# Performance work log

Hardware: AMD Instinct MI355X
Metric: run time of the kernel (lower is better)

## Reference

```python
import jax, jax.numpy as jnp
import numpy as np

B, S_ENC, S_DEC = 256, 1024, 1024
IN, H, OUT = 100, 128, 200
G = 4 * H  # PyTorch LSTM gate rows (i, f, g, o)


def setup_inputs() -> dict:
    key = jax.random.key(0)
    keys = iter(jax.random.split(key, 32))
    w = 1.0 / np.sqrt(H)  # mimic PyTorch LSTM init scale

    def rn(shape, s):
        return jax.random.normal(next(keys), shape, dtype=jnp.float32) * s

    return {
        "x": rn((B, S_ENC, IN), 1.0),
        "y": rn((B, S_DEC, OUT), 1.0),
        "enc_Wih0": rn((G, IN), w), "enc_Whh0": rn((G, H), w),
        "enc_bih0": rn((G,), w), "enc_bhh0": rn((G,), w),
        "enc_Wih1": rn((G, H), w), "enc_Whh1": rn((G, H), w),
        "enc_bih1": rn((G,), w), "enc_bhh1": rn((G,), w),
        "dec_Wih0": rn((G, OUT), w), "dec_Whh0": rn((G, H), w),
        "dec_bih0": rn((G,), w), "dec_bhh0": rn((G,), w),
        "dec_Wih1": rn((G, H), w), "dec_Whh1": rn((G, H), w),
        "dec_bih1": rn((G,), w), "dec_bhh1": rn((G,), w),
        "fc_W": rn((OUT, H), w), "fc_b": rn((OUT,), w),
    }


def lstm_layer(x, h0, c0, Wih, Whh, bih, bhh):
    """Single LSTM layer over full sequence. x: [B,S,D_in] -> [B,S,H], (hT,cT).
    PyTorch gate order: i, f, g, o."""
    # Precompute input projections for all timesteps in one GEMM: [B,S,4H]
    x_proj = jnp.einsum('bsd,gd->bsg', x, Wih) + bih + bhh

    def step(carry, xp_t):
        h, c = carry
        gates = xp_t + h @ Whh.T  # [B,4H]
        i, f, g, o = jnp.split(gates, 4, axis=-1)
        i, f, o = jax.nn.sigmoid(i), jax.nn.sigmoid(f), jax.nn.sigmoid(o)
        g = jnp.tanh(g)
        c = f * c + i * g
        h = o * jnp.tanh(c)
        return (h, c), h

    (hT, cT), hs = jax.lax.scan(step, (h0, c0), x_proj.transpose(1, 0, 2))
    return hs.transpose(1, 0, 2), hT, cT


def lstm_2layer(x, h0_stack, c0_stack, p0, p1):
    """2-layer LSTM. h0_stack/c0_stack: [2,B,H]. p0/p1: (Wih,Whh,bih,bhh)."""
    out0, h0T, c0T = lstm_layer(x, h0_stack[0], c0_stack[0], *p0)
    out1, h1T, c1T = lstm_layer(out0, h0_stack[1], c0_stack[1], *p1)
    hn = jnp.stack([h0T, h1T])
    cn = jnp.stack([c0T, c1T])
    return out1, hn, cn


def reference(x, y,
              enc_Wih0, enc_Whh0, enc_bih0, enc_bhh0,
              enc_Wih1, enc_Whh1, enc_bih1, enc_bhh1,
              dec_Wih0, dec_Whh0, dec_bih0, dec_bhh0,
              dec_Wih1, dec_Whh1, dec_bih1, dec_bhh1,
              fc_W, fc_b):
    b = x.shape[0]
    z = jnp.zeros((2, b, H), dtype=x.dtype)
    # Encoder: zero init state
    _, hn, cn = lstm_2layer(
        x, z, z,
        (enc_Wih0, enc_Whh0, enc_bih0, enc_bhh0),
        (enc_Wih1, enc_Whh1, enc_bih1, enc_bhh1))
    # Teacher-forced decoder: input at step i is y[:, i-1, :], zeros at i=0
    dec_in = jnp.concatenate(
        [jnp.zeros((b, 1, OUT), dtype=y.dtype), y[:, :-1, :]], axis=1)
    dec_out, _, _ = lstm_2layer(
        dec_in, hn, cn,
        (dec_Wih0, dec_Whh0, dec_bih0, dec_bhh0),
        (dec_Wih1, dec_Whh1, dec_bih1, dec_bhh1))
    # Per-step Linear == one batched GEMM over the sequence
    return jnp.einsum('bsh,oh->bso', dec_out, fc_W) + fc_b
```

## Files before the change

kernel.cpp:

```cpp
#include <hip/hip_runtime.h>

#define NB 256
#define HH 128
#define GG 512

#define BM 128
#define BN 128
#define KS 16
#define LPITCH 132

__global__ __launch_bounds__(256, 2) void proj_gemm(
    const float* __restrict__ A, long long lda_b, long long lda_t, int t00, int tsh,
    const float* __restrict__ W,
    const float* __restrict__ b1, const float* __restrict__ b2,
    float* __restrict__ C, long long ldc_b, long long ldc_t, int tC0,
    int CH, int K, int N)
{
  __shared__ float As[KS * LPITCH];
  __shared__ float Ws[KS * LPITCH];

  const int tid = threadIdx.x;
  const int tx = tid & 15;
  const int ty = tid >> 4;

  const long long row0 = (long long)blockIdx.x * BM;
  const int nbase = blockIdx.y * BN;

  const int lr  = tid >> 1;
  const int lks = (tid & 1) * 8;
  const long long lrow = row0 + lr;
  const int lb  = (int)(lrow / CH);
  const int lti = (int)(lrow - (long long)lb * CH);
  const int lt  = t00 + lti + tsh;
  const float* Arow = (lt >= 0) ? (A + (long long)lb * lda_b + (long long)lt * lda_t)
                                : (const float*)nullptr;
  const int ln = nbase + lr;
  const float* Wrow = (ln < N) ? (W + (long long)ln * K) : (const float*)nullptr;

  float acc[8][8];
#pragma unroll
  for (int i = 0; i < 8; ++i)
#pragma unroll
    for (int j = 0; j < 8; ++j) acc[i][j] = 0.f;

  const int nS = (K + KS - 1) / KS;

  float4 ra0 = make_float4(0.f,0.f,0.f,0.f), ra1 = ra0, rw0 = ra0, rw1 = ra0;

  auto loadRegs = [&](int s) {
    const int k0 = s * KS + lks;
    const float4 z = make_float4(0.f, 0.f, 0.f, 0.f);
    ra0 = (Arow && (k0 + 4 <= K)) ? *(const float4*)(Arow + k0)     : z;
    ra1 = (Arow && (k0 + 8 <= K)) ? *(const float4*)(Arow + k0 + 4) : z;
    rw0 = (Wrow && (k0 + 4 <= K)) ? *(const float4*)(Wrow + k0)     : z;
    rw1 = (Wrow && (k0 + 8 <= K)) ? *(const float4*)(Wrow + k0 + 4) : z;
  };

  loadRegs(0);

  for (int s = 0; s < nS; ++s) {
    __syncthreads();
    {
      float av[8] = {ra0.x, ra0.y, ra0.z, ra0.w, ra1.x, ra1.y, ra1.z, ra1.w};
      float wv[8] = {rw0.x, rw0.y, rw0.z, rw0.w, rw1.x, rw1.y, rw1.z, rw1.w};
#pragma unroll
      for (int j = 0; j < 8; ++j) {
        As[(lks + j) * LPITCH + lr] = av[j];
        Ws[(lks + j) * LPITCH + lr] = wv[j];
      }
    }
    __syncthreads();
    if (s + 1 < nS) loadRegs(s + 1);

#pragma unroll
    for (int kk = 0; kk < KS; ++kk) {
      const float* ar = &As[kk * LPITCH];
      const float* wr = &Ws[kk * LPITCH];
      float4 A0 = *(const float4*)(ar + ty * 8);
      float4 A1 = *(const float4*)(ar + ty * 8 + 4);
      float4 W0 = *(const float4*)(wr + tx * 4);
      float4 W1 = *(const float4*)(wr + 64 + tx * 4);
      float am[8] = {A0.x, A0.y, A0.z, A0.w, A1.x, A1.y, A1.z, A1.w};
      float wm[8] = {W0.x, W0.y, W0.z, W0.w, W1.x, W1.y, W1.z, W1.w};
#pragma unroll
      for (int i = 0; i < 8; ++i)
#pragma unroll
        for (int j = 0; j < 8; ++j)
          acc[i][j] = fmaf(am[i], wm[j], acc[i][j]);
    }
  }

  const bool fullN = (nbase + BN <= N);
#pragma unroll
  for (int i = 0; i < 8; ++i) {
    long long row = row0 + ty * 8 + i;
    int bb = (int)(row / CH);
    int ti = (int)(row - (long long)bb * CH);
    float* crow = C + (long long)bb * ldc_b + (long long)(tC0 + ti) * ldc_t;
    if (fullN) {
      int c0 = nbase + tx * 4;
      int c1 = nbase + 64 + tx * 4;
      const float4 bv0 = *(const float4*)(b1 + c0);
      const float4 bv1 = *(const float4*)(b1 + c1);
      float4 v0 = make_float4(acc[i][0] + bv0.x, acc[i][1] + bv0.y,
                              acc[i][2] + bv0.z, acc[i][3] + bv0.w);
      float4 v1 = make_float4(acc[i][4] + bv1.x, acc[i][5] + bv1.y,
                              acc[i][6] + bv1.z, acc[i][7] + bv1.w);
      if (b2) {
        const float4 c20 = *(const float4*)(b2 + c0);
        const float4 c21 = *(const float4*)(b2 + c1);
        v0.x += c20.x; v0.y += c20.y; v0.z += c20.z; v0.w += c20.w;
        v1.x += c21.x; v1.y += c21.y; v1.z += c21.z; v1.w += c21.w;
      }
      *(float4*)(crow + c0) = v0;
      *(float4*)(crow + c1) = v1;
    } else {
#pragma unroll
      for (int j = 0; j < 8; ++j) {
        int col = nbase + ((j < 4) ? (tx * 4 + j) : (64 + tx * 4 + (j - 4)));
        if (col < N) {
          float bv = b1[col];
          if (b2) bv += b2[col];
          crow[col] = acc[i][j] + bv;
        }
      }
    }
  }
}

__device__ __forceinline__ float rl(float v, int l) {
  return __int_as_float(__builtin_amdgcn_readlane(__float_as_int(v), l));
}
__device__ __forceinline__ void barrier_lgkm() {
  asm volatile("s_waitcnt lgkmcnt(0)\n\ts_barrier" ::: "memory");
}
__device__ __forceinline__ float sigm_fast(float x) {
  float e = __expf(-x);
  return __builtin_amdgcn_rcpf(1.f + e);
}
__device__ __forceinline__ float tanh_fast(float x) {
  float e = __expf(2.f * x);
  return fmaf(-2.f, __builtin_amdgcn_rcpf(e + 1.f), 1.f);
}

__global__ __launch_bounds__(512, 2) void lstm_rec(
    const float* __restrict__ xp,
    const float* __restrict__ Whh,
    float* __restrict__ h_state,
    float* __restrict__ c_state,
    float* __restrict__ out_seq,
    int CH, int init)
{
  __shared__ float act_lds[2][GG + 8];

  const int g = threadIdx.x;
  const int b = blockIdx.x;
  const int lane = g & 63;

  float4 w[32];
  {
    const float4* wr4 = (const float4*)(Whh + (long long)g * HH);
#pragma unroll
    for (int i = 0; i < 32; ++i) w[i] = wr4[i];
  }

  float2 hv, cv;
  if (init) {
    hv = make_float2(0.f, 0.f); cv = make_float2(0.f, 0.f);
  } else {
    hv = *(const float2*)&h_state[b * HH + 2 * lane];
    cv = *(const float2*)&c_state[b * HH + 2 * lane];
  }

  const float* xpb = xp + (long long)b * CH * GG + g;
  float xv0 = xpb[0];
  float xv1 = (CH > 1) ? xpb[GG] : 0.f;
  float xv2 = (CH > 2) ? xpb[2 * GG] : 0.f;

  for (int t = 0; t < CH; ++t) {
    float xv3 = (t + 3 < CH) ? xpb[(long long)(t + 3) * GG] : 0.f;

    float a0 = xv0, a1 = 0.f, a2 = 0.f, a3 = 0.f;
#pragma unroll
    for (int q = 0; q < 32; ++q) {
      const float4 wq = w[q];
      const int l0 = 2 * q, l1 = 2 * q + 1;
      a0 = fmaf(rl(hv.x, l0), wq.x, a0);
      a1 = fmaf(rl(hv.y, l0), wq.y, a1);
      a2 = fmaf(rl(hv.x, l1), wq.z, a2);
      a3 = fmaf(rl(hv.y, l1), wq.w, a3);
    }
    const float gate = (a0 + a1) + (a2 + a3);

    const int buf = t & 1;
    const float act = (g >= 2 * HH && g < 3 * HH) ? tanh_fast(gate)
                                                  : sigm_fast(gate);
    act_lds[buf][g + 2 * (g >> 7)] = act;

    barrier_lgkm();

    const int e = 2 * lane;
    const float2 iv = *(const float2*)&act_lds[buf][e];
    const float2 fv = *(const float2*)&act_lds[buf][e + HH + 2];
    const float2 gv = *(const float2*)&act_lds[buf][e + 2 * HH + 4];
    const float2 ov = *(const float2*)&act_lds[buf][e + 3 * HH + 6];
    cv.x = fmaf(fv.x, cv.x, iv.x * gv.x);
    cv.y = fmaf(fv.y, cv.y, iv.y * gv.y);
    hv.x = ov.x * tanh_fast(cv.x);
    hv.y = ov.y * tanh_fast(cv.y);

    if (out_seq && g < 64)
      *(float2*)&out_seq[(long long)b * CH * HH + (long long)t * HH + e] = hv;

    xv0 = xv1; xv1 = xv2; xv2 = xv3;
  }

  if (g < 64) {
    *(float2*)&h_state[b * HH + 2 * lane] = hv;
    *(float2*)&c_state[b * HH + 2 * lane] = cv;
  }
}

extern "C" void kernel_launch(void* const* d_in, const int* in_sizes, int n_in,
                              void* d_out, int out_size, void* d_ws, size_t ws_size,
                              hipStream_t stream)
{
  (void)in_sizes; (void)n_in; (void)out_size;

  const float* x     = (const float*)d_in[0];
  const float* y     = (const float*)d_in[1];
  const float* eWih0 = (const float*)d_in[2];
  const float* eWhh0 = (const float*)d_in[3];
  const float* ebih0 = (const float*)d_in[4];
  const float* ebhh0 = (const float*)d_in[5];
  const float* eWih1 = (const float*)d_in[6];
  const float* eWhh1 = (const float*)d_in[7];
  const float* ebih1 = (const float*)d_in[8];
  const float* ebhh1 = (const float*)d_in[9];
  const float* dWih0 = (const float*)d_in[10];
  const float* dWhh0 = (const float*)d_in[11];
  const float* dbih0 = (const float*)d_in[12];
  const float* dbhh0 = (const float*)d_in[13];
  const float* dWih1 = (const float*)d_in[14];
  const float* dWhh1 = (const float*)d_in[15];
  const float* dbih1 = (const float*)d_in[16];
  const float* dbhh1 = (const float*)d_in[17];
  const float* fcW   = (const float*)d_in[18];
  const float* fcb   = (const float*)d_in[19];
  float* out = (float*)d_out;

  const int S = 1024;

  int CH = 16;
  {
    const int cands[5] = {256, 128, 64, 32, 16};
    for (int i = 0; i < 5; ++i) {
      long long need = (long long)NB * cands[i] * 4LL * (GG + HH + HH)
                     + 4LL * NB * HH * 4
                     + 4096;
      if (need <= (long long)ws_size) { CH = cands[i]; break; }
    }
  }
  const int nchunks = S / CH;

  float* xpb  = (float*)d_ws;
  float* seqA = xpb  + (long long)NB * CH * GG;
  float* seqB = seqA + (long long)NB * CH * HH;
  float* h0s  = seqB + (long long)NB * CH * HH;
  float* c0s  = h0s + NB * HH;
  float* h1s  = c0s + NB * HH;
  float* c1s  = h1s + NB * HH;

  dim3 pgrid((NB * CH) / BM, GG / BN);
  dim3 fgrid((NB * CH) / BM, (200 + BN - 1) / BN);
  dim3 pblk(256);
  dim3 rgrid(NB);
  dim3 rblk(512);

  for (int cidx = 0; cidx < nchunks; ++cidx) {
    int t0 = cidx * CH;
    proj_gemm<<<pgrid, pblk, 0, stream>>>(
        x, (long long)S * 100, 100, t0, 0,
        eWih0, ebih0, ebhh0,
        xpb, (long long)CH * GG, GG, 0, CH, 100, GG);
    lstm_rec<<<rgrid, rblk, 0, stream>>>(xpb, eWhh0, h0s, c0s, seqA, CH, cidx == 0 ? 1 : 0);
    proj_gemm<<<pgrid, pblk, 0, stream>>>(
        seqA, (long long)CH * HH, HH, 0, 0,
        eWih1, ebih1, ebhh1,
        xpb, (long long)CH * GG, GG, 0, CH, HH, GG);
    lstm_rec<<<rgrid, rblk, 0, stream>>>(xpb, eWhh1, h1s, c1s, (float*)nullptr, CH, cidx == 0 ? 1 : 0);
  }

  for (int cidx = 0; cidx < nchunks; ++cidx) {
    int t0 = cidx * CH;
    proj_gemm<<<pgrid, pblk, 0, stream>>>(
        y, (long long)S * 200, 200, t0, -1,
        dWih0, dbih0, dbhh0,
        xpb, (long long)CH * GG, GG, 0, CH, 200, GG);
    lstm_rec<<<rgrid, rblk, 0, stream>>>(xpb, dWhh0, h0s, c0s, seqA, CH, 0);
    proj_gemm<<<pgrid, pblk, 0, stream>>>(
        seqA, (long long)CH * HH, HH, 0, 0,
        dWih1, dbih1, dbhh1,
        xpb, (long long)CH * GG, GG, 0, CH, HH, GG);
    lstm_rec<<<rgrid, rblk, 0, stream>>>(xpb, dWhh1, h1s, c1s, seqB, CH, 0);
    proj_gemm<<<fgrid, pblk, 0, stream>>>(
        seqB, (long long)CH * HH, HH, 0, 0,
        fcW, fcb, (const float*)nullptr,
        out, (long long)S * 200, 200, t0, CH, HH, 200);
  }
}
```

Measured before the change: 9.060 ms.

## Use split-bf16 MFMA for LSTM recurrence with 16 batch rows per block

Replaces the per-batch FP32 readlane/FMA recurrence with a kernel where each block handles 16 batch rows and computes h@Whh^T using bf16 MFMA instructions. The hi/lo bf16 splitting of weights and hidden state (three MFMAs per tile) keeps the result close to fp32. Weights are pre-split once per launch by a small conversion kernel. The hidden state is exchanged through double-buffered LDS. The trade-off is fewer blocks (16 instead of 256), so fewer CUs are used, plus extra split work and some loss of precision.

New measurement: 10.57 ms. 1.17x slower.

```diff
diff --git a/kernel.cpp b/kernel.cpp
--- a/kernel.cpp
+++ b/kernel.cpp
@@ -3,6 +3,9 @@
 #define NB 256
 #define HH 128
 #define GG 512
+
+typedef __attribute__((ext_vector_type(8))) short bf8;
+typedef __attribute__((ext_vector_type(4))) float f32x4;
 
 #define BM 128
 #define BN 128
@@ -128,9 +131,27 @@
   }
 }
 
-__device__ __forceinline__ float rl(float v, int l) {
-  return __int_as_float(__builtin_amdgcn_readlane(__float_as_int(v), l));
-}
+__device__ __forceinline__ unsigned short f2bf(float f) {
+  unsigned int u = __float_as_uint(f);
+  return (unsigned short)((u + 0x7fffu + ((u >> 16) & 1u)) >> 16);
+}
+__device__ __forceinline__ float bf2f(unsigned short h) {
+  return __uint_as_float(((unsigned int)h) << 16);
+}
+
+__global__ void split_bf16(const float* __restrict__ src,
+                           unsigned short* __restrict__ hi,
+                           unsigned short* __restrict__ lo, int n)
+{
+  int i = blockIdx.x * blockDim.x + threadIdx.x;
+  if (i < n) {
+    float v = src[i];
+    unsigned short h = f2bf(v);
+    hi[i] = h;
+    lo[i] = f2bf(v - bf2f(h));
+  }
+}
+
 __device__ __forceinline__ void barrier_lgkm() {
   asm volatile("s_waitcnt lgkmcnt(0)\n\ts_barrier" ::: "memory");
 }
@@ -143,81 +164,153 @@
   return fmaf(-2.f, __builtin_amdgcn_rcpf(e + 1.f), 1.f);
 }
 
-__global__ __launch_bounds__(512, 2) void lstm_rec(
+#define HP 136
+
+__global__ __launch_bounds__(256, 1) void lstm_rec_mfma(
     const float* __restrict__ xp,
-    const float* __restrict__ Whh,
+    const unsigned short* __restrict__ whi,
+    const unsigned short* __restrict__ wlo,
     float* __restrict__ h_state,
     float* __restrict__ c_state,
     float* __restrict__ out_seq,
     int CH, int init)
 {
-  __shared__ float act_lds[2][GG + 8];
-
-  const int g = threadIdx.x;
-  const int b = blockIdx.x;
-  const int lane = g & 63;
-
-  float4 w[32];
-  {
-    const float4* wr4 = (const float4*)(Whh + (long long)g * HH);
-#pragma unroll
-    for (int i = 0; i < 32; ++i) w[i] = wr4[i];
-  }
-
-  float2 hv, cv;
+  __shared__ unsigned short hbuf[2][2][16][HP];
+
+  const int tid  = threadIdx.x;
+  const int lane = tid & 63;
+  const int w    = tid >> 6;
+  const int g4   = lane >> 4;
+  const int bl   = lane & 15;
+  const int bb   = blockIdx.x * 16 + bl;
+  const int hwb  = w * 32 + 4 * g4;
+
+  bf8 WH[8][4], WL[8][4];
+#pragma unroll
+  for (int m = 0; m < 8; ++m) {
+    const int T = m >> 1, s = m & 1;
+    const int grow = T * 128 + w * 32 + s * 16 + bl;
+    const unsigned short* rh = whi + grow * 128 + 4 * g4;
+    const unsigned short* rl = wlo + grow * 128 + 4 * g4;
+#pragma unroll
+    for (int kt = 0; kt < 4; ++kt) {
+      ushort4 a0 = *(const ushort4*)(rh + 32 * kt);
+      ushort4 a1 = *(const ushort4*)(rh + 32 * kt + 16);
+      WH[m][kt] = (bf8){(short)a0.x,(short)a0.y,(short)a0.z,(short)a0.w,
+                        (short)a1.x,(short)a1.y,(short)a1.z,(short)a1.w};
+      ushort4 b0 = *(const ushort4*)(rl + 32 * kt);
+      ushort4 b1 = *(const ushort4*)(rl + 32 * kt + 16);
+      WL[m][kt] = (bf8){(short)b0.x,(short)b0.y,(short)b0.z,(short)b0.w,
+                        (short)b1.x,(short)b1.y,(short)b1.z,(short)b1.w};
+    }
+  }
+
+  float cst[8], hs[8];
   if (init) {
-    hv = make_float2(0.f, 0.f); cv = make_float2(0.f, 0.f);
+#pragma unroll
+    for (int i = 0; i < 8; ++i) { cst[i] = 0.f; hs[i] = 0.f; }
   } else {
-    hv = *(const float2*)&h_state[b * HH + 2 * lane];
-    cv = *(const float2*)&c_state[b * HH + 2 * lane];
-  }
-
-  const float* xpb = xp + (long long)b * CH * GG + g;
-  float xv0 = xpb[0];
-  float xv1 = (CH > 1) ? xpb[GG] : 0.f;
-  float xv2 = (CH > 2) ? xpb[2 * GG] : 0.f;
+#pragma unroll
+    for (int s = 0; s < 2; ++s) {
+      float4 cv = *(const float4*)&c_state[bb * HH + hwb + s * 16];
+      float4 hv = *(const float4*)&h_state[bb * HH + hwb + s * 16];
+      cst[s*4+0]=cv.x; cst[s*4+1]=cv.y; cst[s*4+2]=cv.z; cst[s*4+3]=cv.w;
+      hs [s*4+0]=hv.x; hs [s*4+1]=hv.y; hs [s*4+2]=hv.z; hs [s*4+3]=hv.w;
+    }
+  }
+#pragma unroll
+  for (int s = 0; s < 2; ++s) {
+    ushort4 hi4, lo4;
+    unsigned short h0=f2bf(hs[s*4+0]), h1=f2bf(hs[s*4+1]),
+                   h2=f2bf(hs[s*4+2]), h3=f2bf(hs[s*4+3]);
+    hi4 = (ushort4){h0,h1,h2,h3};
+    lo4 = (ushort4){f2bf(hs[s*4+0]-bf2f(h0)), f2bf(hs[s*4+1]-bf2f(h1)),
+                    f2bf(hs[s*4+2]-bf2f(h2)), f2bf(hs[s*4+3]-bf2f(h3))};
+    *(ushort4*)&hbuf[0][0][bl][hwb + s * 16] = hi4;
+    *(ushort4*)&hbuf[0][1][bl][hwb + s * 16] = lo4;
+  }
+  barrier_lgkm();
+
+  const float* xpt = xp + (long long)bb * CH * GG + w * 32 + 4 * g4;
+  f32x4 xpr[8];
+#pragma unroll
+  for (int m = 0; m < 8; ++m)
+    xpr[m] = *(const f32x4*)(xpt + (m >> 1) * 128 + (m & 1) * 16);
+
+  float* osq = out_seq ? (out_seq + (long long)bb * CH * HH + hwb) : (float*)nullptr;
 
   for (int t = 0; t < CH; ++t) {
-    float xv3 = (t + 3 < CH) ? xpb[(long long)(t + 3) * GG] : 0.f;
-
-    float a0 = xv0, a1 = 0.f, a2 = 0.f, a3 = 0.f;
-#pragma unroll
-    for (int q = 0; q < 32; ++q) {
-      const float4 wq = w[q];
-      const int l0 = 2 * q, l1 = 2 * q + 1;
-      a0 = fmaf(rl(hv.x, l0), wq.x, a0);
-      a1 = fmaf(rl(hv.y, l0), wq.y, a1);
-      a2 = fmaf(rl(hv.x, l1), wq.z, a2);
-      a3 = fmaf(rl(hv.y, l1), wq.w, a3);
-    }
-    const float gate = (a0 + a1) + (a2 + a3);
-
     const int buf = t & 1;
-    const float act = (g >= 2 * HH && g < 3 * HH) ? tanh_fast(gate)
-                                                  : sigm_fast(gate);
-    act_lds[buf][g + 2 * (g >> 7)] = act;
-
+
+    bf8 BH[4], BL[4];
+    const unsigned short* hbH = &hbuf[buf][0][bl][4 * g4];
+    const unsigned short* hbL = &hbuf[buf][1][bl][4 * g4];
+#pragma unroll
+    for (int kt = 0; kt < 4; ++kt) {
+      ushort4 a0 = *(const ushort4*)(hbH + 32 * kt);
+      ushort4 a1 = *(const ushort4*)(hbH + 32 * kt + 16);
+      BH[kt] = (bf8){(short)a0.x,(short)a0.y,(short)a0.z,(short)a0.w,
+                     (short)a1.x,(short)a1.y,(short)a1.z,(short)a1.w};
+      ushort4 b0 = *(const ushort4*)(hbL + 32 * kt);
+      ushort4 b1 = *(const ushort4*)(hbL + 32 * kt + 16);
+      BL[kt] = (bf8){(short)b0.x,(short)b0.y,(short)b0.z,(short)b0.w,
+                     (short)b1.x,(short)b1.y,(short)b1.z,(short)b1.w};
+    }
+
+    f32x4 acc[8];
+#pragma unroll
+    for (int m = 0; m < 8; ++m) acc[m] = xpr[m];
+    if (t + 1 < CH) {
+      const float* xpn = xpt + 512;
+#pragma unroll
+      for (int m = 0; m < 8; ++m)
+        xpr[m] = *(const f32x4*)(xpn + (m >> 1) * 128 + (m & 1) * 16);
+    }
+
+#pragma unroll
+    for (int m = 0; m < 8; ++m)
+#pragma unroll
+      for (int kt = 0; kt < 4; ++kt) {
+        acc[m] = __builtin_amdgcn_mfma_f32_16x16x32_bf16(WH[m][kt], BH[kt], acc[m], 0, 0, 0);
+        acc[m] = __builtin_amdgcn_mfma_f32_16x16x32_bf16(WL[m][kt], BH[kt], acc[m], 0, 0, 0);
+        acc[m] = __builtin_amdgcn_mfma_f32_16x16x32_bf16(WH[m][kt], BL[kt], acc[m], 0, 0, 0);
+      }
+
+#pragma unroll
+    for (int s = 0; s < 2; ++s) {
+#pragma unroll
+      for (int r = 0; r < 4; ++r) {
+        float iv = sigm_fast(acc[0 + s][r]);
+        float fv = sigm_fast(acc[2 + s][r]);
+        float gv = tanh_fast(acc[4 + s][r]);
+        float ov = sigm_fast(acc[6 + s][r]);
+        float c  = fmaf(fv, cst[s * 4 + r], iv * gv);
+        cst[s * 4 + r] = c;
+        hs[s * 4 + r]  = ov * tanh_fast(c);
+      }
+      if (osq) {
+        f32x4 h4 = {hs[s*4+0], hs[s*4+1], hs[s*4+2], hs[s*4+3]};
+        *(f32x4*)(osq + (long long)t * HH + s * 16) = h4;
+      }
+      unsigned short h0=f2bf(hs[s*4+0]), h1=f2bf(hs[s*4+1]),
+                     h2=f2bf(hs[s*4+2]), h3=f2bf(hs[s*4+3]);
+      ushort4 hi4 = (ushort4){h0,h1,h2,h3};
+      ushort4 lo4 = (ushort4){f2bf(hs[s*4+0]-bf2f(h0)), f2bf(hs[s*4+1]-bf2f(h1)),
+                              f2bf(hs[s*4+2]-bf2f(h2)), f2bf(hs[s*4+3]-bf2f(h3))};
+      *(ushort4*)&hbuf[buf ^ 1][0][bl][hwb + s * 16] = hi4;
+      *(ushort4*)&hbuf[buf ^ 1][1][bl][hwb + s * 16] = lo4;
+    }
+
+    xpt += 512;
     barrier_lgkm();
-
-    const int e = 2 * lane;
-    const float2 iv = *(const float2*)&act_lds[buf][e];
-    const float2 fv = *(const float2*)&act_lds[buf][e + HH + 2];
-    const float2 gv = *(const float2*)&act_lds[buf][e + 2 * HH + 4];
-    const float2 ov = *(const float2*)&act_lds[buf][e + 3 * HH + 6];
-    cv.x = fmaf(fv.x, cv.x, iv.x * gv.x);
-    cv.y = fmaf(fv.y, cv.y, iv.y * gv.y);
-    hv.x = ov.x * tanh_fast(cv.x);
-    hv.y = ov.y * tanh_fast(cv.y);
-
-    if (out_seq && g < 64)
-      *(float2*)&out_seq[(long long)b * CH * HH + (long long)t * HH + e] = hv;
-
-    xv0 = xv1; xv1 = xv2; xv2 = xv3;
-  }
-
-  if (g < 64) {
-    *(float2*)&h_state[b * HH + 2 * lane] = hv;
-    *(float2*)&c_state[b * HH + 2 * lane] = cv;
+  }
+
+#pragma unroll
+  for (int s = 0; s < 2; ++s) {
+    f32x4 c4 = {cst[s*4+0], cst[s*4+1], cst[s*4+2], cst[s*4+3]};
+    f32x4 h4 = {hs[s*4+0], hs[s*4+1], hs[s*4+2], hs[s*4+3]};
+    *(f32x4*)&c_state[bb * HH + hwb + s * 16] = c4;
+    *(f32x4*)&h_state[bb * HH + hwb + s * 16] = h4;
   }
 }
 
@@ -250,6 +343,8 @@
   float* out = (float*)d_out;
 
   const int S = 1024;
+  const long long WN = (long long)GG * HH;
+  const long long WSPLIT_BYTES = 4 * 2 * WN * 2;
 
   int CH = 16;
   {
@@ -257,7 +352,7 @@
     for (int i = 0; i < 5; ++i) {
       long long need = (long long)NB * cands[i] * 4LL * (GG + HH + HH)
                      + 4LL * NB * HH * 4
-                     + 4096;
+                     + WSPLIT_BYTES + 4096;
       if (need <= (long long)ws_size) { CH = cands[i]; break; }
     }
   }
@@ -270,12 +365,25 @@
   float* c0s  = h0s + NB * HH;
   float* h1s  = c0s + NB * HH;
   float* c1s  = h1s + NB * HH;
+  unsigned short* wsp = (unsigned short*)(c1s + NB * HH);
+  unsigned short* eW0hi = wsp;             unsigned short* eW0lo = wsp + WN;
+  unsigned short* eW1hi = wsp + 2 * WN;    unsigned short* eW1lo = wsp + 3 * WN;
+  unsigned short* dW0hi = wsp + 4 * WN;    unsigned short* dW0lo = wsp + 5 * WN;
+  unsigned short* dW1hi = wsp + 6 * WN;    unsigned short* dW1lo = wsp + 7 * WN;
+
+  {
+    dim3 pg((WN + 255) / 256), pb(256);
+    split_bf16<<<pg, pb, 0, stream>>>(eWhh0, eW0hi, eW0lo, (int)WN);
+    split_bf16<<<pg, pb, 0, stream>>>(eWhh1, eW1hi, eW1lo, (int)WN);
+    split_bf16<<<pg, pb, 0, stream>>>(dWhh0, dW0hi, dW0lo, (int)WN);
+    split_bf16<<<pg, pb, 0, stream>>>(dWhh1, dW1hi, dW1lo, (int)WN);
+  }
 
   dim3 pgrid((NB * CH) / BM, GG / BN);
   dim3 fgrid((NB * CH) / BM, (200 + BN - 1) / BN);
   dim3 pblk(256);
-  dim3 rgrid(NB);
-  dim3 rblk(512);
+  dim3 rgrid(NB / 16);
+  dim3 rblk(256);
 
   for (int cidx = 0; cidx < nchunks; ++cidx) {
     int t0 = cidx * CH;
@@ -283,12 +391,12 @@
         x, (long long)S * 100, 100, t0, 0,
         eWih0, ebih0, ebhh0,
         xpb, (long long)CH * GG, GG, 0, CH, 100, GG);
-    lstm_rec<<<rgrid, rblk, 0, stream>>>(xpb, eWhh0, h0s, c0s, seqA, CH, cidx == 0 ? 1 : 0);
+    lstm_rec_mfma<<<rgrid, rblk, 0, stream>>>(xpb, eW0hi, eW0lo, h0s, c0s, seqA, CH, cidx == 0 ? 1 : 0);
     proj_gemm<<<pgrid, pblk, 0, stream>>>(
         seqA, (long long)CH * HH, HH, 0, 0,
         eWih1, ebih1, ebhh1,
         xpb, (long long)CH * GG, GG, 0, CH, HH, GG);
-    lstm_rec<<<rgrid, rblk, 0, stream>>>(xpb, eWhh1, h1s, c1s, (float*)nullptr, CH, cidx == 0 ? 1 : 0);
+    lstm_rec_mfma<<<rgrid, rblk, 0, stream>>>(xpb, eW1hi, eW1lo, h1s, c1s, (float*)nullptr, CH, cidx == 0 ? 1 : 0);
   }
 
   for (int cidx = 0; cidx < nchunks; ++cidx) {
@@ -297,12 +405,12 @@
         y, (long long)S * 200, 200, t0, -1,
         dWih0, dbih0, dbhh0,
         xpb, (long long)CH * GG, GG, 0, CH, 200, GG);
-    lstm_rec<<<rgrid, rblk, 0, stream>>>(xpb, dWhh0, h0s, c0s, seqA, CH, 0);
+    lstm_rec_mfma<<<rgrid, rblk, 0, stream>>>(xpb, dW0hi, dW0lo, h0s, c0s, seqA, CH, 0);
     proj_gemm<<<pgrid, pblk, 0, stream>>>(
         seqA, (long long)CH * HH, HH, 0, 0,
         dWih1, dbih1, dbhh1,
         xpb, (long long)CH * GG, GG, 0, CH, HH, GG);
-    lstm_rec<<<rgrid, rblk, 0, stream>>>(xpb, dWhh1, h1s, c1s, seqB, CH, 0);
+    lstm_rec_mfma<<<rgrid, rblk, 0, stream>>>(xpb, dW1hi, dW1lo, h1s, c1s, seqB, CH, 0);
     proj_gemm<<<fgrid, pblk, 0, stream>>>(
         seqB, (long long)CH * HH, HH, 0, 0,
         fcW, fcb, (const float*)nullptr,
```
